# Performance work log

Hardware: AMD Instinct MI355X
Metric: run time of the kernel (lower is better)

Reference implementation:

```python
import jax, jax.numpy as jnp
import numpy as np

B, I, C, J, D, H, W = 16, 32, 8, 10, 16, 6, 6
NUM_ROUTING = 3
EPS = 1e-07


def setup_inputs() -> dict:
    key = jax.random.key(0)
    u_hat = jax.random.normal(key, (B, I, C, J, D, H, W), dtype=jnp.float32)
    # torch module fills bias with 0.1, shape (out_capsules, out_channels, 1, 1)
    bias = jnp.full((J, D, 1, 1), 0.1, dtype=jnp.float32)
    return {"u_hat": u_hat, "bias": bias, "num_routing": NUM_ROUTING}


def _squash(s):
    # Faithful to the source: L1 norm over ALL non-batch dims (not per-capsule L2).
    n1 = jnp.sum(jnp.abs(s), axis=(1, 2, 3, 4), keepdims=True)  # [B,1,1,1,1]
    n1_sq = n1 * n1
    return (n1_sq / (1.0 + n1_sq)) * (s / (n1 + EPS))


def reference(u_hat, bias, num_routing):
    # u_hat: [B,I,C,J,D,H,W]; bias: [J,D,1,1]
    b_ij = jnp.zeros((I, J), dtype=u_hat.dtype)
    v_j = None
    for _ in range(num_routing):
        c_ij = jax.nn.softmax(b_ij, axis=1)  # [I,J]
        # s_j[b,j,d,h,w] = sum_{i,c} c[i,j] * u_hat[b,i,c,j,d,h,w]  (c broadcast over in_channels)
        s_j = jnp.einsum('ij,bicjdhw->bjdhw', c_ij, u_hat) + bias
        v_j = _squash(s_j)  # [B,J,D,H,W]
        # agreement[i,j] = sum over b,c,d,h,w of u_hat * v_j (broadcast over i,c)
        agreement = jnp.einsum('bicjdhw,bjdhw->ij', u_hat, v_j)
        b_ij = b_ij + jax.lax.stop_gradient(agreement)  # torch uses .data (detached)
    return v_j
```

## Files before the change

kernel.cpp:

```cpp
#include <hip/hip_runtime.h>


#define NB   16
#define NI   32
#define NC   8
#define NJ   10
#define ND   16
#define NHW  36
#define NDHW 576
#define NJDHW (NJ * NDHW)
#define NTOT  (NB * NJ * NDHW)
#define EPSV 1e-7f
#define TPB  576


static __device__ __forceinline__ double wave_sum(double v) {
    #pragma unroll
    for (int off = 32; off > 0; off >>= 1) v += __shfl_down(v, off);
    return v;
}

static __device__ __forceinline__ void n1_reduce(float sv, double* slot,
                                                 double* nred ) {
    int tid = threadIdx.x;
    double a = wave_sum((double)fabsf(sv));
    if ((tid & 63) == 0) nred[tid >> 6] = a;
    __syncthreads();
    if (tid == 0) {
        double t = nred[0];
        #pragma unroll
        for (int w = 1; w < 9; ++w) t += nred[w];
        *slot = t;
    }
}

static __device__ __forceinline__ void g_reduce(const float* Uv, float sv,
                                                double* gslot,
                                                double (*gred)[32] ) {
    int tid = threadIdx.x, w = tid >> 6, lane = tid & 63;
    #pragma unroll
    for (int i = 0; i < NI; ++i) {
        double p = wave_sum((double)Uv[i] * (double)sv);
        if (lane == 0) gred[w][i] = p;
    }
    __syncthreads();
    if (tid < NI) {
        double t = gred[0][tid];
        #pragma unroll
        for (int w2 = 1; w2 < 9; ++w2) t += gred[w2][tid];
        gslot[tid] = t;
    }
}

__global__ __launch_bounds__(TPB) void a1_kernel(
    const float4* __restrict__ uh4, const float* __restrict__ bias,
    float4* __restrict__ U2f4, double* __restrict__ n1p, double* __restrict__ Gp)
{
    __shared__ float4  Utile4[NI * 144];
    __shared__ double  nred[9];
    __shared__ double  gred[9][32];

    const int blk = blockIdx.x;
    const int b = blk / NJ, j = blk - b * NJ;
    const int tid = threadIdx.x;

    #pragma unroll
    for (int g = 0; g < 8; ++g) {
        int lin = g * TPB + tid;
        int i  = lin / 144, f4 = lin - i * 144;
        const float4* p = uh4 + ((size_t)(b * NI + i) * NC) * 1440 + j * 144 + f4;
        float4 acc = make_float4(0.f, 0.f, 0.f, 0.f);
        #pragma unroll
        for (int c = 0; c < NC; ++c) {
            float4 v = p[(size_t)c * 1440];
            acc.x += v.x; acc.y += v.y; acc.z += v.z; acc.w += v.w;
        }
        Utile4[lin] = acc;
        U2f4[(size_t)blk * 4608 + lin] = acc;
    }
    __syncthreads();

    const float* Utile = (const float*)Utile4;
    const float cw = 1.0f / 10.0f;
    float Uv[NI];
    float sv = bias[j * ND + tid / NHW];
    #pragma unroll
    for (int i = 0; i < NI; ++i) {
        Uv[i] = Utile[i * NDHW + tid];
        sv += cw * Uv[i];
    }

    n1_reduce(sv, &n1p[blk], nred);
    g_reduce(Uv, sv, &Gp[(size_t)blk * NI], gred);
}

template <int R>
__global__ __launch_bounds__(TPB) void ab_kernel(
    const float* __restrict__ U2, const float* __restrict__ bias,
    const double* __restrict__ n1p, double* __restrict__ Gp,
    double* __restrict__ n1p_out, double* __restrict__ Gp_out,
    float* __restrict__ s)
{
    __shared__ double sc_sh[2][NB];
    __shared__ float  bij_sh[NI * NJ];
    __shared__ float  c_sh[NI];
    __shared__ double nred[9];
    __shared__ double gred[9][32];

    const int blk = blockIdx.x;
    const int b = blk / NJ, j = blk - b * NJ;
    const int tid = threadIdx.x;

    if (tid < R * NB) {
        int rr = tid / NB, bb = tid - rr * NB;
        double n1 = 0.0;
        #pragma unroll
        for (int jj = 0; jj < NJ; ++jj) n1 += n1p[rr * (NB * NJ) + bb * NJ + jj];
        double nsq = n1 * n1;
        sc_sh[rr][bb] = (nsq / (1.0 + nsq)) / (n1 + (double)EPSV);
    }
    __syncthreads();

    if (tid < NI * NJ) {
        int i = tid / NJ, jj = tid - i * NJ;
        double a = 0.0;
        #pragma unroll
        for (int rr = 0; rr < R; ++rr)
            #pragma unroll
            for (int bb = 0; bb < NB; ++bb)
                a += sc_sh[rr][bb] *
                     Gp[(size_t)(rr * NB + bb) * NJ * NI + (size_t)jj * NI + i];
        bij_sh[tid] = (float)a;
    }
    __syncthreads();

    if (tid < NI) {
        float m = -1e30f;
        #pragma unroll
        for (int jj = 0; jj < NJ; ++jj) m = fmaxf(m, bij_sh[tid * NJ + jj]);
        float sum = 0.f;
        #pragma unroll
        for (int jj = 0; jj < NJ; ++jj) sum += expf(bij_sh[tid * NJ + jj] - m);
        c_sh[tid] = expf(bij_sh[tid * NJ + j] - m) / sum;
    }
    __syncthreads();

    const float* u2b = U2 + (size_t)b * 184320 + j * 18432 + tid;
    float Uv[NI];
    float sv = bias[j * ND + tid / NHW];
    #pragma unroll
    for (int i = 0; i < NI; ++i) {
        Uv[i] = u2b[i * 576];
        sv += c_sh[i] * Uv[i];
    }

    if (R == 2) s[(size_t)blk * NDHW + tid] = sv;

    n1_reduce(sv, &n1p_out[b * NJ + j], nred);
    if (R == 1)
        g_reduce(Uv, sv, &Gp_out[(size_t)(b * NJ + j) * NI], gred);
}

__global__ __launch_bounds__(256) void v_kernel(
    const float* __restrict__ s, const double* __restrict__ n1p2,
    float* __restrict__ out)
{
    int e = blockIdx.x * 256 + threadIdx.x;
    int b = e / NJDHW;
    double n1 = 0.0;
    #pragma unroll
    for (int jj = 0; jj < NJ; ++jj) n1 += n1p2[b * NJ + jj];
    float n1f = (float)n1;
    float nsq = n1f * n1f;
    out[e] = (nsq / (1.f + nsq)) * (s[e] / (n1f + EPSV));
}

extern "C" void kernel_launch(void* const* d_in, const int* in_sizes, int n_in,
                              void* d_out, int out_size, void* d_ws, size_t ws_size,
                              hipStream_t stream)
{
    const float* u_hat = (const float*)d_in[0];
    const float* bias  = (const float*)d_in[1];

    float*  U2  = (float*)d_ws;
    float*  s   = U2 + (size_t)NB * NJ * NI * NDHW;
    double* n1p = (double*)(s + NTOT);
    double* Gp  = n1p + 3 * NB * NJ;
    float*  out = (float*)d_out;

    a1_kernel<<<NB * NJ, TPB, 0, stream>>>(
        (const float4*)u_hat, bias, (float4*)U2, n1p, Gp);
    ab_kernel<1><<<NB * NJ, TPB, 0, stream>>>(
        U2, bias, n1p, Gp, n1p + NB * NJ, Gp + NB * NJ * NI, s);
    ab_kernel<2><<<NB * NJ, TPB, 0, stream>>>(
        U2, bias, n1p, Gp, n1p + 2 * NB * NJ, nullptr, s);
    v_kernel<<<NTOT / 256, 256, 0, stream>>>(s, n1p + 2 * NB * NJ, out);
}
```

Measured before the change: 179.1 us.

## Fuse routing iterations into one persistent kernel with grid barriers

Merges the four launches into a single persistent kernel of 160 blocks. Each block keeps its channel-summed U tile in registers across routing iterations and synchronises with a software grid barrier built on atomics. This removes the U2 and s round-trips through global memory and the launch gaps between kernels. In exchange it depends on all 160 blocks being co-resident, and the barrier has a timeout that breaks out of the wait silently, which could give wrong results if blocks are not all scheduled.

```diff
diff --git a/kernel.cpp b/kernel.cpp
--- a/kernel.cpp
+++ b/kernel.cpp
@@ -8,11 +8,11 @@
 #define ND   16
 #define NHW  36
 #define NDHW 576
+#define NBJ  (NB * NJ)
 #define NJDHW (NJ * NDHW)
 #define NTOT  (NB * NJ * NDHW)
 #define EPSV 1e-7f
 #define TPB  576
-
 
 static __device__ __forceinline__ double wave_sum(double v) {
     #pragma unroll
@@ -52,13 +52,47 @@
     }
 }
 
-__global__ __launch_bounds__(TPB) void a1_kernel(
+static __device__ __forceinline__ void grid_barrier(unsigned* bar) {
+    __syncthreads();
+    if (threadIdx.x == 0) {
+        __threadfence();
+        unsigned g = __hip_atomic_load(&bar[1], __ATOMIC_RELAXED,
+                                       __HIP_MEMORY_SCOPE_AGENT);
+        unsigned a = __hip_atomic_fetch_add(&bar[0], 1u, __ATOMIC_RELAXED,
+                                            __HIP_MEMORY_SCOPE_AGENT);
+        if (a == (unsigned)(NBJ - 1)) {
+            __hip_atomic_store(&bar[0], 0u, __ATOMIC_RELAXED,
+                               __HIP_MEMORY_SCOPE_AGENT);
+            __hip_atomic_fetch_add(&bar[1], 1u, __ATOMIC_RELEASE,
+                                   __HIP_MEMORY_SCOPE_AGENT);
+        } else {
+            int guard = 0;
+            while (__hip_atomic_load(&bar[1], __ATOMIC_RELAXED,
+                                     __HIP_MEMORY_SCOPE_AGENT) == g) {
+                __builtin_amdgcn_s_sleep(8);
+                if (++guard > (1 << 17)) break;
+            }
+        }
+        __threadfence();
+    }
+    __syncthreads();
+}
+
+__global__ void init_bar(unsigned* bar) {
+    if (threadIdx.x < 2) bar[threadIdx.x] = 0u;
+}
+
+__global__ __launch_bounds__(TPB) void fused_kernel(
     const float4* __restrict__ uh4, const float* __restrict__ bias,
-    float4* __restrict__ U2f4, double* __restrict__ n1p, double* __restrict__ Gp)
+    double* __restrict__ n1p, double* __restrict__ Gp,
+    unsigned* __restrict__ bar, float* __restrict__ out)
 {
     __shared__ float4  Utile4[NI * 144];
     __shared__ double  nred[9];
     __shared__ double  gred[9][32];
+    __shared__ double  sc_sh[2][NB];
+    __shared__ float   bij_sh[NI * NJ];
+    __shared__ float   c_sh[NI];
 
     const int blk = blockIdx.x;
     const int b = blk / NJ, j = blk - b * NJ;
@@ -76,103 +110,78 @@
             acc.x += v.x; acc.y += v.y; acc.z += v.z; acc.w += v.w;
         }
         Utile4[lin] = acc;
-        U2f4[(size_t)blk * 4608 + lin] = acc;
     }
     __syncthreads();
 
     const float* Utile = (const float*)Utile4;
+    float Uv[NI];
+    #pragma unroll
+    for (int i = 0; i < NI; ++i) Uv[i] = Utile[i * NDHW + tid];
+    const float bv = bias[j * ND + tid / NHW];
+
     const float cw = 1.0f / 10.0f;
-    float Uv[NI];
-    float sv = bias[j * ND + tid / NHW];
-    #pragma unroll
-    for (int i = 0; i < NI; ++i) {
-        Uv[i] = Utile[i * NDHW + tid];
-        sv += cw * Uv[i];
-    }
+    float sv = bv;
+    #pragma unroll
+    for (int i = 0; i < NI; ++i) sv += cw * Uv[i];
 
     n1_reduce(sv, &n1p[blk], nred);
     g_reduce(Uv, sv, &Gp[(size_t)blk * NI], gred);
-}
-
-template <int R>
-__global__ __launch_bounds__(TPB) void ab_kernel(
-    const float* __restrict__ U2, const float* __restrict__ bias,
-    const double* __restrict__ n1p, double* __restrict__ Gp,
-    double* __restrict__ n1p_out, double* __restrict__ Gp_out,
-    float* __restrict__ s)
-{
-    __shared__ double sc_sh[2][NB];
-    __shared__ float  bij_sh[NI * NJ];
-    __shared__ float  c_sh[NI];
-    __shared__ double nred[9];
-    __shared__ double gred[9][32];
-
-    const int blk = blockIdx.x;
-    const int b = blk / NJ, j = blk - b * NJ;
-    const int tid = threadIdx.x;
-
-    if (tid < R * NB) {
-        int rr = tid / NB, bb = tid - rr * NB;
+    grid_barrier(bar);
+
+    for (int R = 1; R <= 2; ++R) {
+        if (tid < R * NB) {
+            int rr = tid / NB, bb = tid - rr * NB;
+            double n1 = 0.0;
+            #pragma unroll
+            for (int jj = 0; jj < NJ; ++jj) n1 += n1p[rr * NBJ + bb * NJ + jj];
+            double nsq = n1 * n1;
+            sc_sh[rr][bb] = (nsq / (1.0 + nsq)) / (n1 + (double)EPSV);
+        }
+        __syncthreads();
+
+        if (tid < NI * NJ) {
+            int i = tid / NJ, jj = tid - i * NJ;
+            double a = 0.0;
+            for (int rr = 0; rr < R; ++rr)
+                #pragma unroll
+                for (int bb = 0; bb < NB; ++bb)
+                    a += sc_sh[rr][bb] *
+                         Gp[(size_t)(rr * NB + bb) * (NJ * NI) + (size_t)jj * NI + i];
+            bij_sh[tid] = (float)a;
+        }
+        __syncthreads();
+
+        if (tid < NI) {
+            float m = -1e30f;
+            #pragma unroll
+            for (int jj = 0; jj < NJ; ++jj) m = fmaxf(m, bij_sh[tid * NJ + jj]);
+            float sum = 0.f;
+            #pragma unroll
+            for (int jj = 0; jj < NJ; ++jj) sum += expf(bij_sh[tid * NJ + jj] - m);
+            c_sh[tid] = expf(bij_sh[tid * NJ + j] - m) / sum;
+        }
+        __syncthreads();
+
+        sv = bv;
+        #pragma unroll
+        for (int i = 0; i < NI; ++i) sv += c_sh[i] * Uv[i];
+
+        n1_reduce(sv, &n1p[R * NBJ + blk], nred);
+        if (R == 1)
+            g_reduce(Uv, sv, &Gp[(size_t)(NBJ + blk) * NI], gred);
+        grid_barrier(bar);
+    }
+
+    if (tid == 0) {
         double n1 = 0.0;
         #pragma unroll
-        for (int jj = 0; jj < NJ; ++jj) n1 += n1p[rr * (NB * NJ) + bb * NJ + jj];
-        double nsq = n1 * n1;
-        sc_sh[rr][bb] = (nsq / (1.0 + nsq)) / (n1 + (double)EPSV);
-    }
-    __syncthreads();
-
-    if (tid < NI * NJ) {
-        int i = tid / NJ, jj = tid - i * NJ;
-        double a = 0.0;
-        #pragma unroll
-        for (int rr = 0; rr < R; ++rr)
-            #pragma unroll
-            for (int bb = 0; bb < NB; ++bb)
-                a += sc_sh[rr][bb] *
-                     Gp[(size_t)(rr * NB + bb) * NJ * NI + (size_t)jj * NI + i];
-        bij_sh[tid] = (float)a;
-    }
-    __syncthreads();
-
-    if (tid < NI) {
-        float m = -1e30f;
-        #pragma unroll
-        for (int jj = 0; jj < NJ; ++jj) m = fmaxf(m, bij_sh[tid * NJ + jj]);
-        float sum = 0.f;
-        #pragma unroll
-        for (int jj = 0; jj < NJ; ++jj) sum += expf(bij_sh[tid * NJ + jj] - m);
-        c_sh[tid] = expf(bij_sh[tid * NJ + j] - m) / sum;
-    }
-    __syncthreads();
-
-    const float* u2b = U2 + (size_t)b * 184320 + j * 18432 + tid;
-    float Uv[NI];
-    float sv = bias[j * ND + tid / NHW];
-    #pragma unroll
-    for (int i = 0; i < NI; ++i) {
-        Uv[i] = u2b[i * 576];
-        sv += c_sh[i] * Uv[i];
-    }
-
-    if (R == 2) s[(size_t)blk * NDHW + tid] = sv;
-
-    n1_reduce(sv, &n1p_out[b * NJ + j], nred);
-    if (R == 1)
-        g_reduce(Uv, sv, &Gp_out[(size_t)(b * NJ + j) * NI], gred);
-}
-
-__global__ __launch_bounds__(256) void v_kernel(
-    const float* __restrict__ s, const double* __restrict__ n1p2,
-    float* __restrict__ out)
-{
-    int e = blockIdx.x * 256 + threadIdx.x;
-    int b = e / NJDHW;
-    double n1 = 0.0;
-    #pragma unroll
-    for (int jj = 0; jj < NJ; ++jj) n1 += n1p2[b * NJ + jj];
-    float n1f = (float)n1;
+        for (int jj = 0; jj < NJ; ++jj) n1 += n1p[2 * NBJ + b * NJ + jj];
+        nred[0] = n1;
+    }
+    __syncthreads();
+    float n1f = (float)nred[0];
     float nsq = n1f * n1f;
-    out[e] = (nsq / (1.f + nsq)) * (s[e] / (n1f + EPSV));
+    out[(size_t)blk * NDHW + tid] = (nsq / (1.f + nsq)) * (sv / (n1f + EPSV));
 }
 
 extern "C" void kernel_launch(void* const* d_in, const int* in_sizes, int n_in,
@@ -181,18 +190,13 @@
 {
     const float* u_hat = (const float*)d_in[0];
     const float* bias  = (const float*)d_in[1];
-
-    float*  U2  = (float*)d_ws;
-    float*  s   = U2 + (size_t)NB * NJ * NI * NDHW;
-    double* n1p = (double*)(s + NTOT);
-    double* Gp  = n1p + 3 * NB * NJ;
-    float*  out = (float*)d_out;
-
-    a1_kernel<<<NB * NJ, TPB, 0, stream>>>(
-        (const float4*)u_hat, bias, (float4*)U2, n1p, Gp);
-    ab_kernel<1><<<NB * NJ, TPB, 0, stream>>>(
-        U2, bias, n1p, Gp, n1p + NB * NJ, Gp + NB * NJ * NI, s);
-    ab_kernel<2><<<NB * NJ, TPB, 0, stream>>>(
-        U2, bias, n1p, Gp, n1p + 2 * NB * NJ, nullptr, s);
-    v_kernel<<<NTOT / 256, 256, 0, stream>>>(s, n1p + 2 * NB * NJ, out);
-}
+    float* out = (float*)d_out;
+
+    double*   n1p = (double*)d_ws;
+    double*   Gp  = n1p + 3 * NBJ;
+    unsigned* bar = (unsigned*)(Gp + 2 * NBJ * NI);
+
+    init_bar<<<1, 64, 0, stream>>>(bar);
+    fused_kernel<<<NBJ, TPB, 0, stream>>>(
+        (const float4*)u_hat, bias, n1p, Gp, bar, out);
+}
```

Measured after the change: 216.1 us. 20.6% more time.

## Split each (b,j) block into three spatial chunks to triple grid size

Applied to the files above, without the earlier changes.

Each (b,j) work block is split into three chunks of 192 spatial elements. That gives 480 blocks of 192 threads instead of 160 blocks of 576 threads, which should spread the work across more of the MI355X's compute units. Partial L1 norms and agreement sums are now stored per chunk, and the downstream kernels sum over the three chunks. This adds more partial-sum reads in the ab and v kernels and changes the floating-point summation order.

```diff
diff --git a/kernel.cpp b/kernel.cpp
--- a/kernel.cpp
+++ b/kernel.cpp
@@ -8,11 +8,14 @@
 #define ND   16
 #define NHW  36
 #define NDHW 576
+#define CK   3
+#define CHK  192
+#define NBJ  (NB * NJ)
+#define NBJC (NBJ * CK)
 #define NJDHW (NJ * NDHW)
 #define NTOT  (NB * NJ * NDHW)
 #define EPSV 1e-7f
-#define TPB  576
-
+#define TPB  192
 
 static __device__ __forceinline__ double wave_sum(double v) {
     #pragma unroll
@@ -26,12 +29,7 @@
     double a = wave_sum((double)fabsf(sv));
     if ((tid & 63) == 0) nred[tid >> 6] = a;
     __syncthreads();
-    if (tid == 0) {
-        double t = nred[0];
-        #pragma unroll
-        for (int w = 1; w < 9; ++w) t += nred[w];
-        *slot = t;
-    }
+    if (tid == 0) slot[0] = (nred[0] + nred[1]) + nred[2];
 }
 
 static __device__ __forceinline__ void g_reduce(const float* Uv, float sv,
@@ -44,31 +42,29 @@
         if (lane == 0) gred[w][i] = p;
     }
     __syncthreads();
-    if (tid < NI) {
-        double t = gred[0][tid];
-        #pragma unroll
-        for (int w2 = 1; w2 < 9; ++w2) t += gred[w2][tid];
-        gslot[tid] = t;
-    }
+    if (tid < NI)
+        gslot[tid] = (gred[0][tid] + gred[1][tid]) + gred[2][tid];
 }
 
 __global__ __launch_bounds__(TPB) void a1_kernel(
     const float4* __restrict__ uh4, const float* __restrict__ bias,
     float4* __restrict__ U2f4, double* __restrict__ n1p, double* __restrict__ Gp)
 {
-    __shared__ float4  Utile4[NI * 144];
-    __shared__ double  nred[9];
-    __shared__ double  gred[9][32];
+    __shared__ float4  Utile4[NI * 48];
+    __shared__ double  nred[3];
+    __shared__ double  gred[3][32];
 
     const int blk = blockIdx.x;
-    const int b = blk / NJ, j = blk - b * NJ;
+    const int bj = blk / CK, ck = blk - bj * CK;
+    const int b = bj / NJ,  j  = bj - b * NJ;
     const int tid = threadIdx.x;
 
     #pragma unroll
     for (int g = 0; g < 8; ++g) {
         int lin = g * TPB + tid;
-        int i  = lin / 144, f4 = lin - i * 144;
-        const float4* p = uh4 + ((size_t)(b * NI + i) * NC) * 1440 + j * 144 + f4;
+        int i  = lin / 48, f4 = lin - i * 48;
+        const float4* p = uh4 + ((size_t)(b * NI + i) * NC) * 1440
+                              + j * 144 + ck * 48 + f4;
         float4 acc = make_float4(0.f, 0.f, 0.f, 0.f);
         #pragma unroll
         for (int c = 0; c < NC; ++c) {
@@ -76,17 +72,17 @@
             acc.x += v.x; acc.y += v.y; acc.z += v.z; acc.w += v.w;
         }
         Utile4[lin] = acc;
-        U2f4[(size_t)blk * 4608 + lin] = acc;
+        U2f4[(size_t)bj * 4608 + i * 144 + ck * 48 + f4] = acc;
     }
     __syncthreads();
 
     const float* Utile = (const float*)Utile4;
     const float cw = 1.0f / 10.0f;
     float Uv[NI];
-    float sv = bias[j * ND + tid / NHW];
+    float sv = bias[j * ND + (ck * CHK + tid) / NHW];
     #pragma unroll
     for (int i = 0; i < NI; ++i) {
-        Uv[i] = Utile[i * NDHW + tid];
+        Uv[i] = Utile[i * CHK + tid];
         sv += cw * Uv[i];
     }
 
@@ -104,33 +100,39 @@
     __shared__ double sc_sh[2][NB];
     __shared__ float  bij_sh[NI * NJ];
     __shared__ float  c_sh[NI];
-    __shared__ double nred[9];
-    __shared__ double gred[9][32];
+    __shared__ double nred[3];
+    __shared__ double gred[3][32];
 
     const int blk = blockIdx.x;
-    const int b = blk / NJ, j = blk - b * NJ;
+    const int bj = blk / CK, ck = blk - bj * CK;
+    const int b = bj / NJ,  j  = bj - b * NJ;
     const int tid = threadIdx.x;
 
     if (tid < R * NB) {
         int rr = tid / NB, bb = tid - rr * NB;
         double n1 = 0.0;
         #pragma unroll
-        for (int jj = 0; jj < NJ; ++jj) n1 += n1p[rr * (NB * NJ) + bb * NJ + jj];
+        for (int jj = 0; jj < NJ; ++jj)
+            #pragma unroll
+            for (int cc = 0; cc < CK; ++cc)
+                n1 += n1p[(size_t)rr * NBJC + (bb * NJ + jj) * CK + cc];
         double nsq = n1 * n1;
         sc_sh[rr][bb] = (nsq / (1.0 + nsq)) / (n1 + (double)EPSV);
     }
     __syncthreads();
 
-    if (tid < NI * NJ) {
-        int i = tid / NJ, jj = tid - i * NJ;
+    for (int e = tid; e < NI * NJ; e += TPB) {
+        int i = e / NJ, jj = e - i * NJ;
         double a = 0.0;
-        #pragma unroll
         for (int rr = 0; rr < R; ++rr)
             #pragma unroll
             for (int bb = 0; bb < NB; ++bb)
-                a += sc_sh[rr][bb] *
-                     Gp[(size_t)(rr * NB + bb) * NJ * NI + (size_t)jj * NI + i];
-        bij_sh[tid] = (float)a;
+                #pragma unroll
+                for (int cc = 0; cc < CK; ++cc)
+                    a += sc_sh[rr][bb] *
+                         Gp[(size_t)rr * (NBJC * NI) +
+                            (size_t)((bb * NJ + jj) * CK + cc) * NI + i];
+        bij_sh[e] = (float)a;
     }
     __syncthreads();
 
@@ -145,20 +147,20 @@
     }
     __syncthreads();
 
-    const float* u2b = U2 + (size_t)b * 184320 + j * 18432 + tid;
+    const float* u2b = U2 + (size_t)bj * 18432 + ck * CHK + tid;
     float Uv[NI];
-    float sv = bias[j * ND + tid / NHW];
+    float sv = bias[j * ND + (ck * CHK + tid) / NHW];
     #pragma unroll
     for (int i = 0; i < NI; ++i) {
-        Uv[i] = u2b[i * 576];
+        Uv[i] = u2b[i * NDHW];
         sv += c_sh[i] * Uv[i];
     }
 
-    if (R == 2) s[(size_t)blk * NDHW + tid] = sv;
-
-    n1_reduce(sv, &n1p_out[b * NJ + j], nred);
+    if (R == 2) s[(size_t)bj * NDHW + ck * CHK + tid] = sv;
+
+    n1_reduce(sv, &n1p_out[blk], nred);
     if (R == 1)
-        g_reduce(Uv, sv, &Gp_out[(size_t)(b * NJ + j) * NI], gred);
+        g_reduce(Uv, sv, &Gp_out[(size_t)blk * NI], gred);
 }
 
 __global__ __launch_bounds__(256) void v_kernel(
@@ -169,7 +171,10 @@
     int b = e / NJDHW;
     double n1 = 0.0;
     #pragma unroll
-    for (int jj = 0; jj < NJ; ++jj) n1 += n1p2[b * NJ + jj];
+    for (int jj = 0; jj < NJ; ++jj)
+        #pragma unroll
+        for (int cc = 0; cc < CK; ++cc)
+            n1 += n1p2[(b * NJ + jj) * CK + cc];
     float n1f = (float)n1;
     float nsq = n1f * n1f;
     out[e] = (nsq / (1.f + nsq)) * (s[e] / (n1f + EPSV));
@@ -185,14 +190,14 @@
     float*  U2  = (float*)d_ws;
     float*  s   = U2 + (size_t)NB * NJ * NI * NDHW;
     double* n1p = (double*)(s + NTOT);
-    double* Gp  = n1p + 3 * NB * NJ;
+    double* Gp  = n1p + 3 * NBJC;
     float*  out = (float*)d_out;
 
-    a1_kernel<<<NB * NJ, TPB, 0, stream>>>(
+    a1_kernel<<<NBJC, TPB, 0, stream>>>(
         (const float4*)u_hat, bias, (float4*)U2, n1p, Gp);
-    ab_kernel<1><<<NB * NJ, TPB, 0, stream>>>(
-        U2, bias, n1p, Gp, n1p + NB * NJ, Gp + NB * NJ * NI, s);
-    ab_kernel<2><<<NB * NJ, TPB, 0, stream>>>(
-        U2, bias, n1p, Gp, n1p + 2 * NB * NJ, nullptr, s);
-    v_kernel<<<NTOT / 256, 256, 0, stream>>>(s, n1p + 2 * NB * NJ, out);
-}
+    ab_kernel<1><<<NBJC, TPB, 0, stream>>>(
+        U2, bias, n1p, Gp, n1p + NBJC, Gp + NBJC * NI, s);
+    ab_kernel<2><<<NBJC, TPB, 0, stream>>>(
+        U2, bias, n1p, Gp, n1p + 2 * NBJC, nullptr, s);
+    v_kernel<<<NTOT / 256, 256, 0, stream>>>(s, n1p + 2 * NBJC, out);
+}
```

After: 209.3 us. +16.9%, slower.

## Fuse last routing pass with squash output and transpose partial-sum layout

Applied to the files above, without the earlier changes.

Merges the third routing iteration and the final squash kernel into one kernel. Each block now recomputes s for all J capsules of its batch, so it can form the full L1 norm locally and write the output directly. This drops one launch and the s buffer round-trip through global memory. In exchange each block reads ten times more U2 data, served from L2. The Gp/n1p partial sums are also stored transposed (b innermost) so the coefficient reduction reads contiguously.

```diff
diff --git a/kernel.cpp b/kernel.cpp
--- a/kernel.cpp
+++ b/kernel.cpp
@@ -8,11 +8,15 @@
 #define ND   16
 #define NHW  36
 #define NDHW 576
-#define NJDHW (NJ * NDHW)
-#define NTOT  (NB * NJ * NDHW)
+#define NBJ  (NB * NJ)
+#define NTOT (NB * NJ * NDHW)
 #define EPSV 1e-7f
 #define TPB  576
-
+#define GP_ITER (NJ * NI * NB)
+#define GP_J    (NI * NB)
+#define GP_I    (NB)
+#define N1_ITER (NB * NJ)
+#define N1_B    (NJ)
 
 static __device__ __forceinline__ double wave_sum(double v) {
     #pragma unroll
@@ -34,9 +38,9 @@
     }
 }
 
-static __device__ __forceinline__ void g_reduce(const float* Uv, float sv,
-                                                double* gslot,
-                                                double (*gred)[32] ) {
+static __device__ __forceinline__ void g_reduce_t(const float* Uv, float sv,
+                                                  double* gbase,
+                                                  double (*gred)[32] ) {
     int tid = threadIdx.x, w = tid >> 6, lane = tid & 63;
     #pragma unroll
     for (int i = 0; i < NI; ++i) {
@@ -48,7 +52,7 @@
         double t = gred[0][tid];
         #pragma unroll
         for (int w2 = 1; w2 < 9; ++w2) t += gred[w2][tid];
-        gslot[tid] = t;
+        gbase[tid * GP_I] = t;
     }
 }
 
@@ -90,18 +94,15 @@
         sv += cw * Uv[i];
     }
 
-    n1_reduce(sv, &n1p[blk], nred);
-    g_reduce(Uv, sv, &Gp[(size_t)blk * NI], gred);
-}
-
-template <int R>
-__global__ __launch_bounds__(TPB) void ab_kernel(
+    n1_reduce(sv, &n1p[b * N1_B + j], nred);
+    g_reduce_t(Uv, sv, Gp + j * GP_J + b, gred);
+}
+
+__global__ __launch_bounds__(TPB) void ab1_kernel(
     const float* __restrict__ U2, const float* __restrict__ bias,
-    const double* __restrict__ n1p, double* __restrict__ Gp,
-    double* __restrict__ n1p_out, double* __restrict__ Gp_out,
-    float* __restrict__ s)
-{
-    __shared__ double sc_sh[2][NB];
+    double* __restrict__ n1p, double* __restrict__ Gp)
+{
+    __shared__ double sc_sh[NB];
     __shared__ float  bij_sh[NI * NJ];
     __shared__ float  c_sh[NI];
     __shared__ double nred[9];
@@ -111,11 +112,71 @@
     const int b = blk / NJ, j = blk - b * NJ;
     const int tid = threadIdx.x;
 
-    if (tid < R * NB) {
-        int rr = tid / NB, bb = tid - rr * NB;
+    if (tid < NB) {
+        const double* np = n1p + tid * N1_B;
         double n1 = 0.0;
         #pragma unroll
-        for (int jj = 0; jj < NJ; ++jj) n1 += n1p[rr * (NB * NJ) + bb * NJ + jj];
+        for (int jj = 0; jj < NJ; ++jj) n1 += np[jj];
+        double nsq = n1 * n1;
+        sc_sh[tid] = (nsq / (1.0 + nsq)) / (n1 + (double)EPSV);
+    }
+    __syncthreads();
+
+    if (tid < NI * NJ) {
+        int i = tid / NJ, jj = tid - i * NJ;
+        const double* g = Gp + jj * GP_J + i * GP_I;
+        double a = 0.0;
+        #pragma unroll
+        for (int bb = 0; bb < NB; ++bb) a += sc_sh[bb] * g[bb];
+        bij_sh[tid] = (float)a;
+    }
+    __syncthreads();
+
+    if (tid < NI) {
+        float m = -1e30f;
+        #pragma unroll
+        for (int jj = 0; jj < NJ; ++jj) m = fmaxf(m, bij_sh[tid * NJ + jj]);
+        float sum = 0.f;
+        #pragma unroll
+        for (int jj = 0; jj < NJ; ++jj) sum += expf(bij_sh[tid * NJ + jj] - m);
+        c_sh[tid] = expf(bij_sh[tid * NJ + j] - m) / sum;
+    }
+    __syncthreads();
+
+    const float* u2b = U2 + (size_t)b * (NJ * NI * NDHW) + j * (NI * NDHW) + tid;
+    float Uv[NI];
+    float sv = bias[j * ND + tid / NHW];
+    #pragma unroll
+    for (int i = 0; i < NI; ++i) {
+        Uv[i] = u2b[i * NDHW];
+        sv += c_sh[i] * Uv[i];
+    }
+
+    n1_reduce(sv, &n1p[N1_ITER + b * N1_B + j], nred);
+    g_reduce_t(Uv, sv, Gp + GP_ITER + j * GP_J + b, gred);
+}
+
+__global__ __launch_bounds__(TPB) void final_kernel(
+    const float* __restrict__ U2, const float* __restrict__ bias,
+    const double* __restrict__ n1p, const double* __restrict__ Gp,
+    float* __restrict__ out)
+{
+    __shared__ double sc_sh[2][NB];
+    __shared__ float  bij_sh[NI * NJ];
+    __shared__ float  c_sh[NI * NJ];
+    __shared__ double nred[9];
+    __shared__ double n1_sh;
+
+    const int blk = blockIdx.x;
+    const int b = blk / NJ, j = blk - b * NJ;
+    const int tid = threadIdx.x;
+
+    if (tid < 2 * NB) {
+        int rr = tid >> 4, bb = tid & 15;
+        const double* np = n1p + rr * N1_ITER + bb * N1_B;
+        double n1 = 0.0;
+        #pragma unroll
+        for (int jj = 0; jj < NJ; ++jj) n1 += np[jj];
         double nsq = n1 * n1;
         sc_sh[rr][bb] = (nsq / (1.0 + nsq)) / (n1 + (double)EPSV);
     }
@@ -124,55 +185,55 @@
     if (tid < NI * NJ) {
         int i = tid / NJ, jj = tid - i * NJ;
         double a = 0.0;
-        #pragma unroll
-        for (int rr = 0; rr < R; ++rr)
+        for (int rr = 0; rr < 2; ++rr) {
+            const double* g = Gp + rr * GP_ITER + jj * GP_J + i * GP_I;
             #pragma unroll
-            for (int bb = 0; bb < NB; ++bb)
-                a += sc_sh[rr][bb] *
-                     Gp[(size_t)(rr * NB + bb) * NJ * NI + (size_t)jj * NI + i];
+            for (int bb = 0; bb < NB; ++bb) a += sc_sh[rr][bb] * g[bb];
+        }
         bij_sh[tid] = (float)a;
     }
     __syncthreads();
 
-    if (tid < NI) {
+    if (tid < NI * NJ) {
+        int i = tid / NJ;
         float m = -1e30f;
         #pragma unroll
-        for (int jj = 0; jj < NJ; ++jj) m = fmaxf(m, bij_sh[tid * NJ + jj]);
+        for (int j2 = 0; j2 < NJ; ++j2) m = fmaxf(m, bij_sh[i * NJ + j2]);
         float sum = 0.f;
         #pragma unroll
-        for (int jj = 0; jj < NJ; ++jj) sum += expf(bij_sh[tid * NJ + jj] - m);
-        c_sh[tid] = expf(bij_sh[tid * NJ + j] - m) / sum;
-    }
-    __syncthreads();
-
-    const float* u2b = U2 + (size_t)b * 184320 + j * 18432 + tid;
-    float Uv[NI];
-    float sv = bias[j * ND + tid / NHW];
-    #pragma unroll
-    for (int i = 0; i < NI; ++i) {
-        Uv[i] = u2b[i * 576];
-        sv += c_sh[i] * Uv[i];
-    }
-
-    if (R == 2) s[(size_t)blk * NDHW + tid] = sv;
-
-    n1_reduce(sv, &n1p_out[b * NJ + j], nred);
-    if (R == 1)
-        g_reduce(Uv, sv, &Gp_out[(size_t)(b * NJ + j) * NI], gred);
-}
-
-__global__ __launch_bounds__(256) void v_kernel(
-    const float* __restrict__ s, const double* __restrict__ n1p2,
-    float* __restrict__ out)
-{
-    int e = blockIdx.x * 256 + threadIdx.x;
-    int b = e / NJDHW;
-    double n1 = 0.0;
-    #pragma unroll
-    for (int jj = 0; jj < NJ; ++jj) n1 += n1p2[b * NJ + jj];
-    float n1f = (float)n1;
+        for (int j2 = 0; j2 < NJ; ++j2) sum += expf(bij_sh[i * NJ + j2] - m);
+        c_sh[tid] = expf(bij_sh[tid] - m) / sum;
+    }
+    __syncthreads();
+
+    const float* ub = U2 + (size_t)b * (NJ * NI * NDHW) + tid;
+    const int drow = tid / NHW;
+    double t = 0.0;
+    float sv_out = 0.f;
+    #pragma unroll 1
+    for (int jj = 0; jj < NJ; ++jj) {
+        const float* up = ub + jj * (NI * NDHW);
+        float sv = bias[jj * ND + drow];
+        #pragma unroll
+        for (int i = 0; i < NI; ++i) sv += c_sh[i * NJ + jj] * up[i * NDHW];
+        t += (double)fabsf(sv);
+        if (jj == j) sv_out = sv;
+    }
+
+    double a = wave_sum(t);
+    if ((tid & 63) == 0) nred[tid >> 6] = a;
+    __syncthreads();
+    if (tid == 0) {
+        double n1 = nred[0];
+        #pragma unroll
+        for (int w = 1; w < 9; ++w) n1 += nred[w];
+        n1_sh = n1;
+    }
+    __syncthreads();
+
+    float n1f = (float)n1_sh;
     float nsq = n1f * n1f;
-    out[e] = (nsq / (1.f + nsq)) * (s[e] / (n1f + EPSV));
+    out[(size_t)blk * NDHW + tid] = (nsq / (1.f + nsq)) * (sv_out / (n1f + EPSV));
 }
 
 extern "C" void kernel_launch(void* const* d_in, const int* in_sizes, int n_in,
@@ -181,18 +242,14 @@
 {
     const float* u_hat = (const float*)d_in[0];
     const float* bias  = (const float*)d_in[1];
+    float* out = (float*)d_out;
 
     float*  U2  = (float*)d_ws;
-    float*  s   = U2 + (size_t)NB * NJ * NI * NDHW;
-    double* n1p = (double*)(s + NTOT);
-    double* Gp  = n1p + 3 * NB * NJ;
-    float*  out = (float*)d_out;
-
-    a1_kernel<<<NB * NJ, TPB, 0, stream>>>(
+    double* n1p = (double*)(U2 + (size_t)NB * NJ * NI * NDHW);
+    double* Gp  = n1p + 2 * N1_ITER;
+
+    a1_kernel<<<NBJ, TPB, 0, stream>>>(
         (const float4*)u_hat, bias, (float4*)U2, n1p, Gp);
-    ab_kernel<1><<<NB * NJ, TPB, 0, stream>>>(
-        U2, bias, n1p, Gp, n1p + NB * NJ, Gp + NB * NJ * NI, s);
-    ab_kernel<2><<<NB * NJ, TPB, 0, stream>>>(
-        U2, bias, n1p, Gp, n1p + 2 * NB * NJ, nullptr, s);
-    v_kernel<<<NTOT / 256, 256, 0, stream>>>(s, n1p + 2 * NB * NJ, out);
-}
+    ab1_kernel<<<NBJ, TPB, 0, stream>>>(U2, bias, n1p, Gp);
+    final_kernel<<<NBJ, TPB, 0, stream>>>(U2, bias, n1p, Gp, out);
+}
```

Result: slower. 185.5 us (+3.6%).
